# Kernel optimization log

Measured on AMD Instinct MI355X. Metric: run time of the kernel, lower is better.

## Reference

```python
import jax, jax.numpy as jnp
import numpy as np

H_IN, W_IN = 128, 128  # sensor grid; region=(1,1), stride=(1,1) -> one RF per pixel


def setup_inputs() -> dict:
    key = jax.random.key(0)
    k1, k2, k3, k4, k5, k6 = jax.random.split(key, 6)
    B, N, C, HID = 8, 2048, 16, 128
    s = 1.0 / np.sqrt(HID)
    features = jax.random.normal(k1, (B, N, C), dtype=jnp.float32)
    coords = jax.random.randint(k2, (B, N, 2), 0, 128, dtype=jnp.int32)  # (x, y)
    w_ih = jax.random.normal(k3, (4 * HID, C), dtype=jnp.float32) * s
    w_hh = jax.random.normal(k4, (4 * HID, HID), dtype=jnp.float32) * s
    b_ih = jax.random.normal(k5, (4 * HID,), dtype=jnp.float32) * s
    b_hh = jax.random.normal(k6, (4 * HID,), dtype=jnp.float32) * s
    return {"features": features, "coords": coords, "w_ih": w_ih,
            "w_hh": w_hh, "b_ih": b_ih, "b_hh": b_hh}


def reference(features, coords, w_ih, w_hh, b_ih, b_hh):
    """MatrixLSTM with 1x1 non-overlapping receptive fields.

    Events (time-ordered along axis 1) are routed to their pixel's RF; a shared
    LSTM is run over each RF's event sequence and the last output per RF is
    scattered into a dense [B, hidden, H, W] map (zeros where no events).
    Implemented as one lax.scan over events with per-RF (h, c) state.
    """
    B, N, C = features.shape
    HID = w_hh.shape[1]
    # coord2idx: raster order y * W + x  -> RF id per event, [B, N]
    rf = coords[:, :, 1].astype(jnp.int32) * W_IN + coords[:, :, 0].astype(jnp.int32)
    bidx = jnp.arange(B)
    bias = b_ih + b_hh

    def step(carry, inp):
        h_all, c_all = carry              # [B, num_rf, HID] each
        x_t, rf_t = inp                   # [B, C], [B]
        h_prev = h_all[bidx, rf_t]        # gather per-RF state, [B, HID]
        c_prev = c_all[bidx, rf_t]
        gates = x_t @ w_ih.T + h_prev @ w_hh.T + bias  # [B, 4*HID]
        i, f, g, o = jnp.split(gates, 4, axis=-1)       # torch LSTM gate order
        i = jax.nn.sigmoid(i)
        f = jax.nn.sigmoid(f)
        g = jnp.tanh(g)
        o = jax.nn.sigmoid(o)
        c_new = f * c_prev + i * g
        h_new = o * jnp.tanh(c_new)
        h_all = h_all.at[bidx, rf_t].set(h_new)        # scatter back
        c_all = c_all.at[bidx, rf_t].set(c_new)
        return (h_all, c_all), None

    h0 = jnp.zeros((B, H_IN * W_IN, HID), features.dtype)
    c0 = jnp.zeros_like(h0)
    (h_all, _), _ = jax.lax.scan(step, (h0, c0),
                                 (features.transpose(1, 0, 2), rf.T))
    # final h per RF == LSTM output at each RF's last event; zeros if no events
    return h_all.reshape(B, H_IN, W_IN, HID).transpose(0, 3, 1, 2)
```

## Files before the change

### kernel.cpp

```cpp
#include <hip/hip_runtime.h>
#include <hip/hip_bf16.h>
#include <math.h>

#define B 8
#define N 2048
#define C 16
#define HID 128
#define NRF 16384
#define MAXLEN 8
#define MAXCH 2048

__device__ __forceinline__ float sigf(float x) { return 1.f / (1.f + expf(-x)); }

__global__ __launch_bounds__(1024) void k_pre(
    const int* __restrict__ coords, const float* __restrict__ w_ih,
    const float* __restrict__ w_hh, const float* __restrict__ b_ih,
    const float* __restrict__ b_hh, float* __restrict__ w_ih_T,
    float* __restrict__ w_hh_T, float* __restrict__ biassum,
    int* __restrict__ map, int* __restrict__ cnt, int* __restrict__ chainrf,
    int* __restrict__ chainlen, int* __restrict__ slots) {
    int tid = threadIdx.x;
    if (blockIdx.x < 8) {
        int bb = blockIdx.x;
        __shared__ int cnt_l[NRF];
        __shared__ int nch_l;
#pragma unroll
        for (int i = 0; i < 16; i++) cnt_l[tid + 1024 * i] = 0;
        if (tid == 0) nch_l = 0;
#pragma unroll
        for (int i = 0; i < 16; i++) map[bb * NRF + tid + 1024 * i] = -1;
        __syncthreads();
        int n0 = tid, n1 = tid + 1024;
        int2 c0 = ((const int2*)coords)[bb * N + n0];
        int2 c1 = ((const int2*)coords)[bb * N + n1];
        int rf0 = c0.y * 128 + c0.x;
        int rf1 = c1.y * 128 + c1.x;
        int pos0 = atomicAdd(&cnt_l[rf0], 1);
        int pos1 = atomicAdd(&cnt_l[rf1], 1);
        if (pos0 < MAXLEN) slots[((size_t)bb * NRF + rf0) * MAXLEN + pos0] = n0;
        if (pos1 < MAXLEN) slots[((size_t)bb * NRF + rf1) * MAXLEN + pos1] = n1;
        __syncthreads();
#pragma unroll
        for (int e = 0; e < 2; e++) {
            int rf = e ? rf1 : rf0;
            int pos = e ? pos1 : pos0;
            if (pos == 0) {
                int j = atomicAdd(&nch_l, 1);
                int len = cnt_l[rf];
                if (len > MAXLEN) len = MAXLEN;
                chainrf[bb * MAXCH + j] = rf;
                chainlen[bb * MAXCH + j] = len;
                map[bb * NRF + rf] = j;
            }
        }
        __syncthreads();
        if (tid == 0) cnt[bb] = nch_l;
    } else {
        int i = (blockIdx.x - 8) * 1024 + tid;
        if (i < C * 512) {
            int c = i >> 9, j = i & 511;
            w_ih_T[i] = w_ih[j * C + c];
        }
        if (i < HID * 512) {
            int k = i >> 9, j = i & 511;
            w_hh_T[i] = w_hh[j * HID + k];
        }
        if (i < 512) biassum[i] = b_ih[i] + b_hh[i];
    }
}

__global__ __launch_bounds__(256) void k_phase(
    const float* __restrict__ features, const float* __restrict__ w_ih_T,
    const float* __restrict__ w_hh_T, const float* __restrict__ biassum,
    const int* __restrict__ cnt, const int* __restrict__ chainrf,
    const int* __restrict__ chainlen, int* __restrict__ slots,
    float* __restrict__ hfin) {
    int tid = threadIdx.x;
    int bb = blockIdx.x >> 8;
    int slot0 = (blockIdx.x & 255) * 8;
    __shared__ float ls_w[C * 512];
    __shared__ float ls_b[512];
    __shared__ float h_st[8][HID], c_st[8][HID];
    __shared__ float g_s[512];
    __shared__ float x_s[16];
    __shared__ int l_idx[8], l_len[8], l_ev0[8];
    int nc = cnt[bb];
    if (tid < 8) {
        int j = slot0 + tid;
        int idx = bb * MAXCH + j;
        if (j < nc) {
            int len = chainlen[idx];
            int* sl = slots + ((size_t)bb * NRF + chainrf[idx]) * MAXLEN;
            int ev0;
            if (len >= 2) {
                int ev[MAXLEN];
#pragma unroll
                for (int t = 0; t < MAXLEN; t++) {
                    int v = sl[t];
                    ev[t] = (t < len) ? v : 0x7fffffff;
                }
#pragma unroll
                for (int a = 0; a < MAXLEN; a++)
#pragma unroll
                    for (int q = 0; q < MAXLEN - 1; q++) {
                        int u = ev[q], v = ev[q + 1];
                        ev[q] = min(u, v);
                        ev[q + 1] = max(u, v);
                    }
                for (int t = 0; t < len; t++) sl[t] = ev[t];
                ev0 = ev[0];
            } else {
                ev0 = sl[0];
            }
            l_idx[tid] = idx; l_len[tid] = len; l_ev0[tid] = ev0;
        } else {
            l_idx[tid] = -1; l_len[tid] = 0;
        }
    }
    for (int i = tid; i < C * 128; i += 256)
        ((float4*)ls_w)[i] = ((const float4*)w_ih_T)[i];
    ls_b[tid] = biassum[tid];
    ls_b[tid + 256] = biassum[tid + 256];
    __syncthreads();
    int w = tid >> 6, lane = tid & 63;
#pragma unroll
    for (int s2 = 0; s2 < 2; s2++) {
        int s = 2 * w + s2;
        int idx = l_idx[s];
        if (idx < 0) continue;
        int len = l_len[s];
        int n = l_ev0[s];
        float f = 0.f;
        if (lane < 16) f = features[((size_t)(bb * N + n)) * C + lane];
        float ai0 = ls_b[lane],       ai1 = ls_b[lane + 64];
        float ag0 = ls_b[lane + 256], ag1 = ls_b[lane + 320];
        float ao0 = ls_b[lane + 384], ao1 = ls_b[lane + 448];
#pragma unroll
        for (int c2 = 0; c2 < 16; c2++) {
            float xv = __shfl(f, c2, 64);
            ai0 += ls_w[c2 * 512 + lane]       * xv;
            ai1 += ls_w[c2 * 512 + lane + 64]  * xv;
            ag0 += ls_w[c2 * 512 + lane + 256] * xv;
            ag1 += ls_w[c2 * 512 + lane + 320] * xv;
            ao0 += ls_w[c2 * 512 + lane + 384] * xv;
            ao1 += ls_w[c2 * 512 + lane + 448] * xv;
        }
        float c0 = sigf(ai0) * tanhf(ag0);
        float c1 = sigf(ai1) * tanhf(ag1);
        float h0 = sigf(ao0) * tanhf(c0);
        float h1 = sigf(ao1) * tanhf(c1);
        if (len == 1) {
            hfin[(size_t)idx * HID + lane] = h0;
            hfin[(size_t)idx * HID + lane + 64] = h1;
        } else {
            h_st[s][lane] = h0; h_st[s][lane + 64] = h1;
            c_st[s][lane] = c0; c_st[s][lane + 64] = c1;
        }
    }
    for (int s = 0; s < 8; s++) {
        int len = l_len[s];
        if (len < 2) continue;
        int idx = l_idx[s];
        const int* sl = slots + ((size_t)bb * NRF + chainrf[idx]) * MAXLEN;
        for (int t = 1; t < len; t++) {
            __syncthreads();
            if (tid < 16)
                x_s[tid] = features[((size_t)(bb * N + sl[t])) * C + tid];
            __syncthreads();
            float a0 = ls_b[tid], a1 = ls_b[tid + 256];
#pragma unroll
            for (int c2 = 0; c2 < 16; c2++) {
                float xv = x_s[c2];
                a0 += ls_w[c2 * 512 + tid] * xv;
                a1 += ls_w[c2 * 512 + tid + 256] * xv;
            }
#pragma unroll 8
            for (int k = 0; k < 128; k++) {
                float hv = h_st[s][k];
                a0 += w_hh_T[k * 512 + tid] * hv;
                a1 += w_hh_T[k * 512 + tid + 256] * hv;
            }
            g_s[tid] = a0;
            g_s[tid + 256] = a1;
            __syncthreads();
            if (tid < 128) {
                float ig = sigf(g_s[tid]);
                float fg = sigf(g_s[tid + 128]);
                float gg = tanhf(g_s[tid + 256]);
                float og = sigf(g_s[tid + 384]);
                float cn = fg * c_st[s][tid] + ig * gg;
                c_st[s][tid] = cn;
                h_st[s][tid] = og * tanhf(cn);
            }
        }
        __syncthreads();
        if (tid < 128) hfin[(size_t)idx * HID + tid] = h_st[s][tid];
    }
}

__global__ __launch_bounds__(256) void k_scatter(
    const float* __restrict__ hfin, const int* __restrict__ map,
    float* __restrict__ out) {
    int b = blockIdx.x >> 7;
    int y = blockIdx.x & 127;
    int t = threadIdx.x;
    int xq = t & 31;
    int hg = t >> 5;
    const int4* mrow = (const int4*)(map + b * NRF + y * 128);
    int4 kk = mrow[xq];
    const float* hb = hfin + (size_t)b * MAXCH * HID;
#pragma unroll
    for (int hh = 0; hh < 16; hh++) {
        int hid = hg * 16 + hh;
        float4 v;
        v.x = (kk.x < 0) ? 0.f : hb[kk.x * HID + hid];
        v.y = (kk.y < 0) ? 0.f : hb[kk.y * HID + hid];
        v.z = (kk.z < 0) ? 0.f : hb[kk.z * HID + hid];
        v.w = (kk.w < 0) ? 0.f : hb[kk.w * HID + hid];
        *(float4*)(out + ((((size_t)b * HID + hid) * 128 + y) * 128) + xq * 4) = v;
    }
}

extern "C" void kernel_launch(void* const* d_in, const int* in_sizes, int n_in,
                              void* d_out, int out_size, void* d_ws, size_t ws_size,
                              hipStream_t stream) {
    const float* features = (const float*)d_in[0];
    const int*   coords   = (const int*)d_in[1];
    const float* w_ih     = (const float*)d_in[2];
    const float* w_hh     = (const float*)d_in[3];
    const float* b_ih     = (const float*)d_in[4];
    const float* b_hh     = (const float*)d_in[5];
    float* out = (float*)d_out;

    char* ws = (char*)d_ws;
    float* w_ih_T   = (float*)(ws + 0);
    float* w_hh_T   = (float*)(ws + 32768);
    float* biassum  = (float*)(ws + 294912);
    int*   map      = (int*)(ws + 296960);
    int*   cnt      = (int*)(ws + 821248);
    int*   chainrf  = (int*)(ws + 821312);
    int*   chainlen = (int*)(ws + 886848);
    int*   slots    = (int*)(ws + 952384);
    float* hfin     = (float*)(ws + 5146688);

    k_pre<<<dim3(81), dim3(1024), 0, stream>>>(
        coords, w_ih, w_hh, b_ih, b_hh, w_ih_T, w_hh_T, biassum,
        map, cnt, chainrf, chainlen, slots);
    k_phase<<<dim3(2048), dim3(256), 0, stream>>>(
        features, w_ih_T, w_hh_T, biassum, cnt, chainrf, chainlen, slots, hfin);
    k_scatter<<<dim3(B * 128), dim3(256), 0, stream>>>(hfin, map, out);
}
```

Before: 139.5 us.

## Split first-event gates from multi-event recurrence into separate kernels with compacted work list

Moves the per-chain event sort into the preprocessing kernel and builds a compacted list of RFs that have two or more events. First-step gate computation runs in its own kernel over 16 chains per block and writes h and c to global memory. A new recurrence kernel handles only multi-event chains, one chain per block at a time, with split accumulators and a prefetch of the next event's features. This removes the serial per-block loop over chains that idled most threads, at the cost of an extra launch and a global round trip for h/c state.

```diff
diff --git a/kernel.cpp b/kernel.cpp
--- a/kernel.cpp
+++ b/kernel.cpp
@@ -17,16 +17,17 @@
     const float* __restrict__ w_hh, const float* __restrict__ b_ih,
     const float* __restrict__ b_hh, float* __restrict__ w_ih_T,
     float* __restrict__ w_hh_T, float* __restrict__ biassum,
-    int* __restrict__ map, int* __restrict__ cnt, int* __restrict__ chainrf,
-    int* __restrict__ chainlen, int* __restrict__ slots) {
+    int* __restrict__ map, int* __restrict__ cnt, int* __restrict__ mcnt,
+    int* __restrict__ chainpk, int* __restrict__ mlist,
+    int* __restrict__ slots) {
     int tid = threadIdx.x;
     if (blockIdx.x < 8) {
         int bb = blockIdx.x;
         __shared__ int cnt_l[NRF];
-        __shared__ int nch_l;
+        __shared__ int nch_l, nmul_l;
 #pragma unroll
         for (int i = 0; i < 16; i++) cnt_l[tid + 1024 * i] = 0;
-        if (tid == 0) nch_l = 0;
+        if (tid == 0) { nch_l = 0; nmul_l = 0; }
 #pragma unroll
         for (int i = 0; i < 16; i++) map[bb * NRF + tid + 1024 * i] = -1;
         __syncthreads();
@@ -48,13 +49,35 @@
                 int j = atomicAdd(&nch_l, 1);
                 int len = cnt_l[rf];
                 if (len > MAXLEN) len = MAXLEN;
-                chainrf[bb * MAXCH + j] = rf;
-                chainlen[bb * MAXCH + j] = len;
                 map[bb * NRF + rf] = j;
-            }
-        }
-        __syncthreads();
-        if (tid == 0) cnt[bb] = nch_l;
+                int* sl = slots + ((size_t)bb * NRF + rf) * MAXLEN;
+                int ev[MAXLEN];
+#pragma unroll
+                for (int t = 0; t < MAXLEN; t++) {
+                    int v = sl[t];
+                    ev[t] = (t < len) ? v : 0x7fffffff;
+                }
+#pragma unroll
+                for (int a = 0; a < MAXLEN; a++)
+#pragma unroll
+                    for (int q = 0; q < MAXLEN - 1; q++) {
+                        int u = ev[q], v = ev[q + 1];
+                        ev[q] = min(u, v);
+                        ev[q + 1] = max(u, v);
+                    }
+                if (len >= 2) {
+                    for (int t = 0; t < len; t++) sl[t] = ev[t];
+                    int m = atomicAdd(&nmul_l, 1);
+                    if (m < 1024) mlist[bb * 1024 + m] = j | (rf << 11);
+                }
+                chainpk[bb * MAXCH + j] = ev[0] | (len << 11);
+            }
+        }
+        __syncthreads();
+        if (tid == 0) {
+            cnt[bb] = nch_l;
+            mcnt[bb] = (nmul_l > 1024) ? 1024 : nmul_l;
+        }
     } else {
         int i = (blockIdx.x - 8) * 1024 + tid;
         if (i < C * 512) {
@@ -69,53 +92,21 @@
     }
 }
 
-__global__ __launch_bounds__(256) void k_phase(
+__global__ __launch_bounds__(256) void k_gate0(
     const float* __restrict__ features, const float* __restrict__ w_ih_T,
-    const float* __restrict__ w_hh_T, const float* __restrict__ biassum,
-    const int* __restrict__ cnt, const int* __restrict__ chainrf,
-    const int* __restrict__ chainlen, int* __restrict__ slots,
-    float* __restrict__ hfin) {
+    const float* __restrict__ biassum, const int* __restrict__ cnt,
+    const int* __restrict__ chainpk, float* __restrict__ hfin,
+    float* __restrict__ cfin) {
     int tid = threadIdx.x;
-    int bb = blockIdx.x >> 8;
-    int slot0 = (blockIdx.x & 255) * 8;
+    int bb = blockIdx.x >> 7;
+    int slot0 = (blockIdx.x & 127) * 16;
     __shared__ float ls_w[C * 512];
     __shared__ float ls_b[512];
-    __shared__ float h_st[8][HID], c_st[8][HID];
-    __shared__ float g_s[512];
-    __shared__ float x_s[16];
-    __shared__ int l_idx[8], l_len[8], l_ev0[8];
+    __shared__ int l_pk[16];
     int nc = cnt[bb];
-    if (tid < 8) {
+    if (tid < 16) {
         int j = slot0 + tid;
-        int idx = bb * MAXCH + j;
-        if (j < nc) {
-            int len = chainlen[idx];
-            int* sl = slots + ((size_t)bb * NRF + chainrf[idx]) * MAXLEN;
-            int ev0;
-            if (len >= 2) {
-                int ev[MAXLEN];
-#pragma unroll
-                for (int t = 0; t < MAXLEN; t++) {
-                    int v = sl[t];
-                    ev[t] = (t < len) ? v : 0x7fffffff;
-                }
-#pragma unroll
-                for (int a = 0; a < MAXLEN; a++)
-#pragma unroll
-                    for (int q = 0; q < MAXLEN - 1; q++) {
-                        int u = ev[q], v = ev[q + 1];
-                        ev[q] = min(u, v);
-                        ev[q + 1] = max(u, v);
-                    }
-                for (int t = 0; t < len; t++) sl[t] = ev[t];
-                ev0 = ev[0];
-            } else {
-                ev0 = sl[0];
-            }
-            l_idx[tid] = idx; l_len[tid] = len; l_ev0[tid] = ev0;
-        } else {
-            l_idx[tid] = -1; l_len[tid] = 0;
-        }
+        l_pk[tid] = (j < nc) ? chainpk[bb * MAXCH + j] : -1;
     }
     for (int i = tid; i < C * 128; i += 256)
         ((float4*)ls_w)[i] = ((const float4*)w_ih_T)[i];
@@ -123,21 +114,25 @@
     ls_b[tid + 256] = biassum[tid + 256];
     __syncthreads();
     int w = tid >> 6, lane = tid & 63;
-#pragma unroll
-    for (int s2 = 0; s2 < 2; s2++) {
-        int s = 2 * w + s2;
-        int idx = l_idx[s];
-        if (idx < 0) continue;
-        int len = l_len[s];
-        int n = l_ev0[s];
-        float f = 0.f;
-        if (lane < 16) f = features[((size_t)(bb * N + n)) * C + lane];
+    int pk[4];
+    float f[4];
+#pragma unroll
+    for (int s2 = 0; s2 < 4; s2++) {
+        pk[s2] = l_pk[w * 4 + s2];
+        f[s2] = 0.f;
+        if (pk[s2] >= 0 && lane < 16)
+            f[s2] = features[((size_t)(bb * N + (pk[s2] & 2047))) * C + lane];
+    }
+#pragma unroll
+    for (int s2 = 0; s2 < 4; s2++) {
+        if (pk[s2] < 0) continue;
+        int len = pk[s2] >> 11;
         float ai0 = ls_b[lane],       ai1 = ls_b[lane + 64];
         float ag0 = ls_b[lane + 256], ag1 = ls_b[lane + 320];
         float ao0 = ls_b[lane + 384], ao1 = ls_b[lane + 448];
 #pragma unroll
         for (int c2 = 0; c2 < 16; c2++) {
-            float xv = __shfl(f, c2, 64);
+            float xv = __shfl(f[s2], c2, 64);
             ai0 += ls_w[c2 * 512 + lane]       * xv;
             ai1 += ls_w[c2 * 512 + lane + 64]  * xv;
             ag0 += ls_w[c2 * 512 + lane + 256] * xv;
@@ -149,52 +144,78 @@
         float c1 = sigf(ai1) * tanhf(ag1);
         float h0 = sigf(ao0) * tanhf(c0);
         float h1 = sigf(ao1) * tanhf(c1);
-        if (len == 1) {
-            hfin[(size_t)idx * HID + lane] = h0;
-            hfin[(size_t)idx * HID + lane + 64] = h1;
-        } else {
-            h_st[s][lane] = h0; h_st[s][lane + 64] = h1;
-            c_st[s][lane] = c0; c_st[s][lane + 64] = c1;
-        }
-    }
-    for (int s = 0; s < 8; s++) {
-        int len = l_len[s];
-        if (len < 2) continue;
-        int idx = l_idx[s];
-        const int* sl = slots + ((size_t)bb * NRF + chainrf[idx]) * MAXLEN;
+        size_t idx = (size_t)(bb * MAXCH + slot0 + w * 4 + s2);
+        hfin[idx * HID + lane] = h0;
+        hfin[idx * HID + lane + 64] = h1;
+        if (len >= 2) {
+            cfin[idx * HID + lane] = c0;
+            cfin[idx * HID + lane + 64] = c1;
+        }
+    }
+}
+
+__global__ __launch_bounds__(256) void k_recur(
+    const float* __restrict__ features, const float* __restrict__ w_ih_T,
+    const float* __restrict__ w_hh_T, const float* __restrict__ biassum,
+    const int* __restrict__ chainpk, const int* __restrict__ mcnt,
+    const int* __restrict__ mlist, const int* __restrict__ slots,
+    float* __restrict__ hfin, const float* __restrict__ cfin) {
+    int tid = threadIdx.x;
+    int bb = blockIdx.x >> 7;
+    int m0 = blockIdx.x & 127;
+    int M = mcnt[bb];
+    if (m0 >= M) return;
+    __shared__ float h_s[HID], c_s[HID];
+    __shared__ float x_s[16];
+    __shared__ float g_s[512];
+    float bs0 = biassum[tid], bs1 = biassum[tid + 256];
+    for (int m = m0; m < M; m += 128) {
+        int e = mlist[bb * 1024 + m];
+        int j = e & 2047;
+        int rf = e >> 11;
+        size_t idx = (size_t)(bb * MAXCH + j);
+        int len = chainpk[bb * MAXCH + j] >> 11;
+        const int* sl = slots + ((size_t)bb * NRF + rf) * MAXLEN;
+        if (tid < 16) x_s[tid] = features[((size_t)(bb * N + sl[1])) * C + tid];
+        if (tid < 128) {
+            h_s[tid] = hfin[idx * HID + tid];
+            c_s[tid] = cfin[idx * HID + tid];
+        }
+        __syncthreads();
         for (int t = 1; t < len; t++) {
-            __syncthreads();
-            if (tid < 16)
-                x_s[tid] = features[((size_t)(bb * N + sl[t])) * C + tid];
-            __syncthreads();
-            float a0 = ls_b[tid], a1 = ls_b[tid + 256];
+            float a0 = bs0, a1 = bs1, b0 = 0.f, b1 = 0.f;
 #pragma unroll
             for (int c2 = 0; c2 < 16; c2++) {
                 float xv = x_s[c2];
-                a0 += ls_w[c2 * 512 + tid] * xv;
-                a1 += ls_w[c2 * 512 + tid + 256] * xv;
+                a0 += w_ih_T[c2 * 512 + tid] * xv;
+                a1 += w_ih_T[c2 * 512 + tid + 256] * xv;
             }
 #pragma unroll 8
-            for (int k = 0; k < 128; k++) {
-                float hv = h_st[s][k];
-                a0 += w_hh_T[k * 512 + tid] * hv;
-                a1 += w_hh_T[k * 512 + tid + 256] * hv;
-            }
-            g_s[tid] = a0;
-            g_s[tid + 256] = a1;
+            for (int k = 0; k < 128; k += 2) {
+                float h0 = h_s[k], h1 = h_s[k + 1];
+                a0 += w_hh_T[k * 512 + tid] * h0;
+                a1 += w_hh_T[k * 512 + tid + 256] * h0;
+                b0 += w_hh_T[(k + 1) * 512 + tid] * h1;
+                b1 += w_hh_T[(k + 1) * 512 + tid + 256] * h1;
+            }
+            g_s[tid] = a0 + b0;
+            g_s[tid + 256] = a1 + b1;
             __syncthreads();
             if (tid < 128) {
                 float ig = sigf(g_s[tid]);
                 float fg = sigf(g_s[tid + 128]);
                 float gg = tanhf(g_s[tid + 256]);
                 float og = sigf(g_s[tid + 384]);
-                float cn = fg * c_st[s][tid] + ig * gg;
-                c_st[s][tid] = cn;
-                h_st[s][tid] = og * tanhf(cn);
-            }
-        }
-        __syncthreads();
-        if (tid < 128) hfin[(size_t)idx * HID + tid] = h_st[s][tid];
+                float cn = fg * c_s[tid] + ig * gg;
+                c_s[tid] = cn;
+                h_s[tid] = og * tanhf(cn);
+            }
+            if (tid < 16 && t + 1 < len)
+                x_s[tid] = features[((size_t)(bb * N + sl[t + 1])) * C + tid];
+            __syncthreads();
+        }
+        if (tid < 128) hfin[idx * HID + tid] = h_s[tid];
+        __syncthreads();
     }
 }
 
@@ -238,15 +259,20 @@
     float* biassum  = (float*)(ws + 294912);
     int*   map      = (int*)(ws + 296960);
     int*   cnt      = (int*)(ws + 821248);
-    int*   chainrf  = (int*)(ws + 821312);
-    int*   chainlen = (int*)(ws + 886848);
-    int*   slots    = (int*)(ws + 952384);
-    float* hfin     = (float*)(ws + 5146688);
+    int*   mcnt     = (int*)(ws + 821312);
+    int*   chainpk  = (int*)(ws + 821376);
+    int*   mlist    = (int*)(ws + 886912);
+    int*   slots    = (int*)(ws + 919680);
+    float* hfin     = (float*)(ws + 5113984);
+    float* cfin     = (float*)(ws + 13502592);
 
     k_pre<<<dim3(81), dim3(1024), 0, stream>>>(
         coords, w_ih, w_hh, b_ih, b_hh, w_ih_T, w_hh_T, biassum,
-        map, cnt, chainrf, chainlen, slots);
-    k_phase<<<dim3(2048), dim3(256), 0, stream>>>(
-        features, w_ih_T, w_hh_T, biassum, cnt, chainrf, chainlen, slots, hfin);
+        map, cnt, mcnt, chainpk, mlist, slots);
+    k_gate0<<<dim3(1024), dim3(256), 0, stream>>>(
+        features, w_ih_T, biassum, cnt, chainpk, hfin, cfin);
+    k_recur<<<dim3(1024), dim3(256), 0, stream>>>(
+        features, w_ih_T, w_hh_T, biassum, chainpk, mcnt, mlist, slots,
+        hfin, cfin);
     k_scatter<<<dim3(B * 128), dim3(256), 0, stream>>>(hfin, map, out);
 }
```

After: 138.3 us. No clear change (-0.9%).
